# Kernel tuning notes

Hardware: AMD Instinct MI355X
Metric: run time of the kernel (lower is better)

The kernel has to match this reference:

```python
import jax, jax.numpy as jnp
import numpy as np

D_MODEL, D_FF, N_EXPERTS, TOP_K = 1024, 4096, 8, 2
B, S = 2, 2048


def setup_inputs() -> dict:
    key = jax.random.key(0)
    ks = jax.random.split(key, 7)
    scale = 0.02
    return {
        "x": jax.random.normal(ks[0], (B, S, D_MODEL), dtype=jnp.float32),
        "W1": jax.random.normal(ks[1], (N_EXPERTS, D_MODEL, D_FF), dtype=jnp.float32) * scale,
        "b1": jnp.zeros((N_EXPERTS, D_FF), dtype=jnp.float32),
        "W2": jax.random.normal(ks[2], (N_EXPERTS, D_FF, D_MODEL), dtype=jnp.float32) * scale,
        "b2": jnp.zeros((N_EXPERTS, D_MODEL), dtype=jnp.float32),
        "Wg": jax.random.normal(ks[3], (D_MODEL, N_EXPERTS), dtype=jnp.float32) * scale,
        "bg": jnp.zeros((N_EXPERTS,), dtype=jnp.float32),
    }


def reference(x, W1, b1, W2, b2, Wg, bg):
    # x: [B, S, d_model]
    Bx, Sx, d = x.shape
    E = W1.shape[0]
    # Gate + top-k routing (softmax over the top-k scores, as in the torch code)
    logits = jnp.einsum("bsd,de->bse", x, Wg) + bg            # [B,S,E]
    topk_scores, topk_idx = jax.lax.top_k(logits, TOP_K)       # [B,S,K]
    topk_scores = jax.nn.softmax(topk_scores, axis=-1)

    tokens = x.reshape(-1, d)                                  # [T,d]
    idx_flat = topk_idx.reshape(-1, TOP_K)                     # [T,K]
    sc_flat = topk_scores.reshape(-1, TOP_K)                   # [T,K]
    # Per-token combine weight for each expert: sum_k score_k * 1[idx_k == e]
    comb = (jax.nn.one_hot(idx_flat, E, dtype=x.dtype) * sc_flat[..., None]).sum(axis=1)  # [T,E]

    # Dense grouped expert MLP (zero combine weight kills non-selected experts)
    h = jnp.einsum("td,edf->etf", tokens, W1) + b1[:, None, :]  # [E,T,d_ff]
    even = (jnp.arange(E) % 2 == 0)[:, None, None]
    # torch nn.GELU default = exact (erf); odd experts use SiLU
    a = jnp.where(even, jax.nn.gelu(h, approximate=False), jax.nn.silu(h))
    y = jnp.einsum("etf,efd->etd", a, W2) + b2[:, None, :]      # [E,T,d_model]
    out = jnp.einsum("te,etd->td", comb, y)                     # [T,d_model]
    # Dropout is identity in eval mode
    return out.reshape(Bx, Sx, d)
```

## Files before the change

kernel.cpp:

```cpp
#include <hip/hip_runtime.h>
#include <stdint.h>

#define T_TOK 4096
#define DM 1024
#define DF 4096
#define NE 8

typedef __attribute__((ext_vector_type(8))) short bf16x8;
typedef __attribute__((ext_vector_type(4))) float f32x4;

__device__ __forceinline__ float b2f(unsigned short u) {
    union { unsigned int i; float f; } v; v.i = ((unsigned int)u) << 16; return v.f;
}
__device__ __forceinline__ unsigned short f2b(float f) {
    unsigned int i = __float_as_uint(f);
    unsigned int r = (i + 0x7FFFu + ((i >> 16) & 1u)) >> 16;
    return (unsigned short)r;
}
__device__ __forceinline__ void load_lds16(const void* g, void* l) {
    __builtin_amdgcn_global_load_lds((__attribute__((address_space(1))) void*)(g),
                                     (__attribute__((address_space(3))) void*)(l), 16, 0, 0);
}

__global__ __launch_bounds__(256) void detect_kernel(const unsigned short* __restrict__ xu,
                                                     int* __restrict__ flag) {
    const int i = (blockIdx.x * 256 + threadIdx.x) * 4;
    uint2 v = *(const uint2*)&xu[i];
    unsigned int a = v.x, b = v.y;
    int found = 0;
    if (((a >> 7)  & 0xFF) == 0xFF) found = 1;
    if (((a >> 23) & 0xFF) == 0xFF) found = 1;
    if (((b >> 7)  & 0xFF) == 0xFF) found = 1;
    if (((b >> 23) & 0xFF) == 0xFF) found = 1;
    if (__ballot(found) != 0 && (threadIdx.x & 63) == 0) atomicOr(flag, 1);
}

__global__ __launch_bounds__(256) void convx_kernel(const void* __restrict__ xin,
                                                    const int* __restrict__ flag,
                                                    unsigned short* __restrict__ xb) {
    const size_t i = ((size_t)blockIdx.x * 256 + threadIdx.x) * 8;
    if (*flag) {
        const float* xf = (const float*)xin + i;
        float4 a = *(const float4*)xf;
        float4 b = *(const float4*)(xf + 4);
        alignas(16) unsigned short t[8] = { f2b(a.x), f2b(a.y), f2b(a.z), f2b(a.w),
                                            f2b(b.x), f2b(b.y), f2b(b.z), f2b(b.w) };
        *(uint4*)(xb + i) = *(const uint4*)t;
    } else {
        *(uint4*)(xb + i) = *(const uint4*)((const unsigned short*)xin + i);
    }
}

__global__ void convf_kernel(const void* __restrict__ src, const int* __restrict__ flag,
                             float* __restrict__ dst, int n) {
    int i = blockIdx.x * 256 + threadIdx.x;
    if (i < n) dst[i] = (*flag) ? ((const float*)src)[i] : b2f(((const unsigned short*)src)[i]);
}

__global__ __launch_bounds__(256) void transpose_kernel(const void* __restrict__ in,
                                                        unsigned short* __restrict__ out,
                                                        int R, int C, const int* __restrict__ flag) {
    __shared__ unsigned short tile[64][65];
    const int isf = *flag;
    const size_t base = (size_t)blockIdx.z * R * C;
    const int r0 = blockIdx.y * 64, c0 = blockIdx.x * 64;
    const int lr = threadIdx.x >> 2;
    const int lc = (threadIdx.x & 3) * 16;
    if (isf) {
        const float* src = (const float*)in + base + (size_t)(r0 + lr) * C + c0 + lc;
#pragma unroll
        for (int q = 0; q < 4; q++) {
            float4 v = *(const float4*)(src + q * 4);
            tile[lr][lc + q * 4 + 0] = f2b(v.x);
            tile[lr][lc + q * 4 + 1] = f2b(v.y);
            tile[lr][lc + q * 4 + 2] = f2b(v.z);
            tile[lr][lc + q * 4 + 3] = f2b(v.w);
        }
    } else {
        const unsigned short* src = (const unsigned short*)in + base + (size_t)(r0 + lr) * C + c0 + lc;
#pragma unroll
        for (int q = 0; q < 2; q++) {
            uint4 v = *(const uint4*)(src + q * 8);
            unsigned int w[4] = { v.x, v.y, v.z, v.w };
#pragma unroll
            for (int j = 0; j < 4; j++) {
                tile[lr][lc + q * 8 + 2 * j]     = (unsigned short)(w[j] & 0xffff);
                tile[lr][lc + q * 8 + 2 * j + 1] = (unsigned short)(w[j] >> 16);
            }
        }
    }
    __syncthreads();
    const int oc = threadIdx.x >> 2;
    const int oj = (threadIdx.x & 3) * 16;
    alignas(16) unsigned short tmp[16];
#pragma unroll
    for (int j = 0; j < 16; j++) tmp[j] = tile[oj + j][oc];
    unsigned short* dst = out + base + (size_t)(c0 + oc) * R + r0 + oj;
    *(uint4*)(dst) = *(const uint4*)(tmp);
    *(uint4*)(dst + 8) = *(const uint4*)(tmp + 8);
}

__global__ __launch_bounds__(256) void gate_kernel(
    const void* __restrict__ x, const void* __restrict__ Wg, const void* __restrict__ bg,
    const int* __restrict__ flag, int* __restrict__ cnt,
    int* __restrict__ tok_e, float* __restrict__ tok_s) {
    const int isf = *flag;
    const int wave = threadIdx.x >> 6, lane = threadIdx.x & 63;
    const int t = blockIdx.x * 4 + wave;
    float p[8] = {0.f,0.f,0.f,0.f,0.f,0.f,0.f,0.f};
    if (isf) {
        const float* xr = (const float*)x + (size_t)t * DM;
        const float* wg = (const float*)Wg;
        for (int i = lane; i < DM; i += 64) {
            float xv = xr[i];
            float4 a = *(const float4*)(wg + (size_t)i * 8);
            float4 b = *(const float4*)(wg + (size_t)i * 8 + 4);
            p[0] += xv * a.x; p[1] += xv * a.y; p[2] += xv * a.z; p[3] += xv * a.w;
            p[4] += xv * b.x; p[5] += xv * b.y; p[6] += xv * b.z; p[7] += xv * b.w;
        }
    } else {
        const unsigned short* xr = (const unsigned short*)x + (size_t)t * DM;
        const unsigned short* wg = (const unsigned short*)Wg;
        for (int i = lane; i < DM; i += 64) {
            float xv = b2f(xr[i]);
            uint4 wv = *(const uint4*)(wg + (size_t)i * 8);
            p[0] += xv * b2f((unsigned short)(wv.x & 0xffff));
            p[1] += xv * b2f((unsigned short)(wv.x >> 16));
            p[2] += xv * b2f((unsigned short)(wv.y & 0xffff));
            p[3] += xv * b2f((unsigned short)(wv.y >> 16));
            p[4] += xv * b2f((unsigned short)(wv.z & 0xffff));
            p[5] += xv * b2f((unsigned short)(wv.z >> 16));
            p[6] += xv * b2f((unsigned short)(wv.w & 0xffff));
            p[7] += xv * b2f((unsigned short)(wv.w >> 16));
        }
    }
    for (int off = 32; off > 0; off >>= 1)
        for (int e = 0; e < 8; e++) p[e] += __shfl_down(p[e], off);
    if (lane == 0) {
        for (int e = 0; e < 8; e++)
            p[e] += isf ? ((const float*)bg)[e] : b2f(((const unsigned short*)bg)[e]);
        int e0 = 0;
        for (int e = 1; e < 8; e++) if (p[e] > p[e0]) e0 = e;
        int e1 = (e0 == 0) ? 1 : 0;
        for (int e = 0; e < 8; e++) if (e != e0 && p[e] > p[e1]) e1 = e;
        float z = expf(p[e1] - p[e0]);
        float s0 = 1.f / (1.f + z);
        tok_e[2 * t] = e0; tok_e[2 * t + 1] = e1;
        tok_s[2 * t] = s0; tok_s[2 * t + 1] = z * s0;
        atomicAdd(&cnt[e0], 1); atomicAdd(&cnt[e1], 1);
    }
}

__global__ void scan_kernel(const int* __restrict__ cnt, int* __restrict__ offs) {
    if (threadIdx.x == 0) {
        int s = 0;
        for (int e = 0; e < NE; e++) { offs[e] = s; s += cnt[e]; }
    }
}

__global__ __launch_bounds__(256) void place_kernel(
    const int* __restrict__ tok_e, const int* __restrict__ offs, int* __restrict__ cnt2,
    int* __restrict__ tok_list, int* __restrict__ slot_of) {
    const int t = blockIdx.x * 256 + threadIdx.x;
    for (int k = 0; k < 2; k++) {
        int e = tok_e[2 * t + k];
        int slot = atomicAdd(&cnt2[e], 1);
        int idx = offs[e] + slot;
        tok_list[idx] = t;
        slot_of[2 * t + k] = idx;
    }
}

__global__ __launch_bounds__(256) void gemm1_kernel(
    const unsigned short* __restrict__ xb, const unsigned short* __restrict__ W1T,
    const float* __restrict__ b1f, const int* __restrict__ tok_list,
    const int* __restrict__ offs, const int* __restrict__ cnt,
    unsigned short* __restrict__ act) {
    const int e = blockIdx.z, by = blockIdx.y, bx = blockIdx.x;
    const int ne = cnt[e];
    if (by * 128 >= ne) return;
    const int off_e = offs[e];
    __shared__ unsigned short Asm[128 * 32];
    __shared__ unsigned short Bsm[128 * 32];
    __shared__ int toks[128];
    const int tid = threadIdx.x, w = tid >> 6, lane = tid & 63;
    if (tid < 128) {
        int r = by * 128 + tid;
        toks[tid] = tok_list[off_e + (r < ne ? r : ne - 1)];
    }
    __syncthreads();
    const int arow0 = w * 16 + (lane >> 2);
    const int acol = (lane & 3) * 8;
    const int tok0 = toks[arow0], tok1 = toks[arow0 + 64];
    const unsigned short* gA0 = xb + (size_t)tok0 * DM + acol;
    const unsigned short* gA1 = xb + (size_t)tok1 * DM + acol;
    const unsigned short* Wte = W1T + (size_t)e * DF * DM;
    const unsigned short* gB0 = Wte + (size_t)(bx * 128 + arow0) * DM + acol;
    const unsigned short* gB1 = gB0 + (size_t)64 * DM;
    unsigned short* ldsA0 = &Asm[(w) * 16 * 32];
    unsigned short* ldsA1 = &Asm[(w + 4) * 16 * 32];
    unsigned short* ldsB0 = &Bsm[(w) * 16 * 32];
    unsigned short* ldsB1 = &Bsm[(w + 4) * 16 * 32];
    f32x4 acc[4][4] = {};
    const int mb = (w >> 1) * 64, nb = (w & 1) * 64;
    for (int kk = 0; kk < DM; kk += 32) {
        load_lds16(gA0 + kk, ldsA0);
        load_lds16(gA1 + kk, ldsA1);
        load_lds16(gB0 + kk, ldsB0);
        load_lds16(gB1 + kk, ldsB1);
        __syncthreads();
        bf16x8 af[4], bfv[4];
#pragma unroll
        for (int i = 0; i < 4; i++)
            af[i] = *(const bf16x8*)&Asm[(mb + i * 16 + (lane & 15)) * 32 + (lane >> 4) * 8];
#pragma unroll
        for (int j = 0; j < 4; j++)
            bfv[j] = *(const bf16x8*)&Bsm[(nb + j * 16 + (lane & 15)) * 32 + (lane >> 4) * 8];
#pragma unroll
        for (int i = 0; i < 4; i++)
#pragma unroll
            for (int j = 0; j < 4; j++)
                acc[i][j] = __builtin_amdgcn_mfma_f32_16x16x32_bf16(af[i], bfv[j], acc[i][j], 0, 0, 0);
        __syncthreads();
    }
    const bool even_e = (e & 1) == 0;
    const float* b1e = b1f + (size_t)e * DF + bx * 128;
#pragma unroll
    for (int i = 0; i < 4; i++) {
#pragma unroll
        for (int r = 0; r < 4; r++) {
            int m = mb + i * 16 + ((lane >> 4) * 4) + r;
            int grow = by * 128 + m;
            if (grow < ne) {
                unsigned short* dst = act + (size_t)(off_e + grow) * DF + bx * 128;
#pragma unroll
                for (int j = 0; j < 4; j++) {
                    int n = nb + j * 16 + (lane & 15);
                    float h = acc[i][j][r] + b1e[n];
                    float a;
                    if (even_e) a = 0.5f * h * (1.f + erff(h * 0.70710678118654752f));
                    else        a = h / (1.f + expf(-h));
                    dst[n] = f2b(a);
                }
            }
        }
    }
}

__global__ __launch_bounds__(256) void gemm2_kernel(
    const unsigned short* __restrict__ act, const unsigned short* __restrict__ W2T,
    const float* __restrict__ b2f, const int* __restrict__ offs,
    const int* __restrict__ cnt, float* __restrict__ yall) {
    const int e = blockIdx.z, by = blockIdx.y, bx = blockIdx.x;
    const int ne = cnt[e];
    if (by * 128 >= ne) return;
    const int off_e = offs[e];
    __shared__ unsigned short Asm[128 * 32];
    __shared__ unsigned short Bsm[128 * 32];
    const int tid = threadIdx.x, w = tid >> 6, lane = tid & 63;
    const int arow0 = w * 16 + (lane >> 2);
    const int acol = (lane & 3) * 8;
    int r0 = by * 128 + arow0;       if (r0 > ne - 1) r0 = ne - 1;
    int r1 = by * 128 + arow0 + 64;  if (r1 > ne - 1) r1 = ne - 1;
    const unsigned short* gA0 = act + (size_t)(off_e + r0) * DF + acol;
    const unsigned short* gA1 = act + (size_t)(off_e + r1) * DF + acol;
    const unsigned short* Wte = W2T + (size_t)e * DM * DF;
    const unsigned short* gB0 = Wte + (size_t)(bx * 128 + arow0) * DF + acol;
    const unsigned short* gB1 = gB0 + (size_t)64 * DF;
    unsigned short* ldsA0 = &Asm[(w) * 16 * 32];
    unsigned short* ldsA1 = &Asm[(w + 4) * 16 * 32];
    unsigned short* ldsB0 = &Bsm[(w) * 16 * 32];
    unsigned short* ldsB1 = &Bsm[(w + 4) * 16 * 32];
    f32x4 acc[4][4] = {};
    const int mb = (w >> 1) * 64, nb = (w & 1) * 64;
    for (int kk = 0; kk < DF; kk += 32) {
        load_lds16(gA0 + kk, ldsA0);
        load_lds16(gA1 + kk, ldsA1);
        load_lds16(gB0 + kk, ldsB0);
        load_lds16(gB1 + kk, ldsB1);
        __syncthreads();
        bf16x8 af[4], bfv[4];
#pragma unroll
        for (int i = 0; i < 4; i++)
            af[i] = *(const bf16x8*)&Asm[(mb + i * 16 + (lane & 15)) * 32 + (lane >> 4) * 8];
#pragma unroll
        for (int j = 0; j < 4; j++)
            bfv[j] = *(const bf16x8*)&Bsm[(nb + j * 16 + (lane & 15)) * 32 + (lane >> 4) * 8];
#pragma unroll
        for (int i = 0; i < 4; i++)
#pragma unroll
            for (int j = 0; j < 4; j++)
                acc[i][j] = __builtin_amdgcn_mfma_f32_16x16x32_bf16(af[i], bfv[j], acc[i][j], 0, 0, 0);
        __syncthreads();
    }
    const float* b2e = b2f + (size_t)e * DM + bx * 128;
#pragma unroll
    for (int i = 0; i < 4; i++) {
#pragma unroll
        for (int r = 0; r < 4; r++) {
            int m = mb + i * 16 + ((lane >> 4) * 4) + r;
            int grow = by * 128 + m;
            if (grow < ne) {
                float* dst = yall + (size_t)(off_e + grow) * DM + bx * 128;
#pragma unroll
                for (int j = 0; j < 4; j++) {
                    int n = nb + j * 16 + (lane & 15);
                    dst[n] = acc[i][j][r] + b2e[n];
                }
            }
        }
    }
}

__global__ __launch_bounds__(256) void combine_kernel(
    const float* __restrict__ yall, const int* __restrict__ slot_of,
    const float* __restrict__ tok_s, void* __restrict__ out, const int* __restrict__ flag) {
    const int t = blockIdx.x;
    const int c = threadIdx.x * 4;
    const int s0i = slot_of[2 * t], s1i = slot_of[2 * t + 1];
    const float w0 = tok_s[2 * t], w1 = tok_s[2 * t + 1];
    float4 a = *(const float4*)&yall[(size_t)s0i * DM + c];
    float4 b = *(const float4*)&yall[(size_t)s1i * DM + c];
    float4 r;
    r.x = w0 * a.x + w1 * b.x;
    r.y = w0 * a.y + w1 * b.y;
    r.z = w0 * a.z + w1 * b.z;
    r.w = w0 * a.w + w1 * b.w;
    if (*flag) {
        *(float4*)((float*)out + (size_t)t * DM + c) = r;
    } else {
        ushort4 o;
        o.x = f2b(r.x); o.y = f2b(r.y); o.z = f2b(r.z); o.w = f2b(r.w);
        *(ushort4*)((unsigned short*)out + (size_t)t * DM + c) = o;
    }
}

extern "C" void kernel_launch(void* const* d_in, const int* in_sizes, int n_in,
                              void* d_out, int out_size, void* d_ws, size_t ws_size,
                              hipStream_t stream) {
    (void)in_sizes; (void)n_in; (void)out_size; (void)ws_size;
    const void* x  = d_in[0];
    const void* W1 = d_in[1];
    const void* b1 = d_in[2];
    const void* W2 = d_in[3];
    const void* b2 = d_in[4];
    const void* Wg = d_in[5];
    const void* bg = d_in[6];

    uint8_t* wsb = (uint8_t*)d_ws;
    int* ip = (int*)wsb;
    int* flag  = ip;
    int* cnt   = ip + 8;
    int* cnt2  = ip + 16;
    int* offs  = ip + 24;
    int* tok_e = ip + 32;
    float* tok_s  = (float*)(tok_e + 2 * T_TOK);
    int* tok_list = (int*)(tok_s + 2 * T_TOK);
    int* slot_of  = tok_list + 2 * T_TOK;
    size_t head = (size_t)((uint8_t*)(slot_of + 2 * T_TOK) - wsb);
    head = (head + 255) & ~(size_t)255;
    float* b1f = (float*)(wsb + head);
    float* b2f = b1f + (size_t)NE * DF;
    unsigned short* xb  = (unsigned short*)(b2f + (size_t)NE * DM);
    unsigned short* W1T = xb + (size_t)T_TOK * DM;
    unsigned short* W2T = W1T + (size_t)NE * DM * DF;
    unsigned short* actb = W2T + (size_t)NE * DM * DF;
    float* yall = (float*)W1T;

    hipMemsetAsync(ip, 0, 128, stream);
    detect_kernel<<<256, 256, 0, stream>>>((const unsigned short*)x, flag);
    convx_kernel<<<(T_TOK * DM) / 2048, 256, 0, stream>>>(x, flag, xb);
    convf_kernel<<<(NE * DF) / 256, 256, 0, stream>>>(b1, flag, b1f, NE * DF);
    convf_kernel<<<(NE * DM) / 256, 256, 0, stream>>>(b2, flag, b2f, NE * DM);
    transpose_kernel<<<dim3(DF / 64, DM / 64, NE), 256, 0, stream>>>(W1, W1T, DM, DF, flag);
    transpose_kernel<<<dim3(DM / 64, DF / 64, NE), 256, 0, stream>>>(W2, W2T, DF, DM, flag);
    gate_kernel<<<T_TOK / 4, 256, 0, stream>>>(x, Wg, bg, flag, cnt, tok_e, tok_s);
    scan_kernel<<<1, 64, 0, stream>>>(cnt, offs);
    place_kernel<<<T_TOK / 256, 256, 0, stream>>>(tok_e, offs, cnt2, tok_list, slot_of);
    gemm1_kernel<<<dim3(DF / 128, T_TOK / 128, NE), 256, 0, stream>>>(xb, W1T, b1f, tok_list, offs, cnt, actb);
    gemm2_kernel<<<dim3(DM / 128, T_TOK / 128, NE), 256, 0, stream>>>(actb, W2T, b2f, offs, cnt, yall);
    combine_kernel<<<T_TOK, 256, 0, stream>>>(yall, slot_of, tok_s, d_out, flag);
}
```

Baseline: 762.5 us.

## Double-buffer LDS tiles, swizzle LDS layout, and use fast activation approximations

Both expert GEMM kernels now use two LDS buffers, issuing the next K-slice's global-to-LDS loads before computing the current one, so memory latency can overlap MFMA work and one barrier per iteration is dropped. The column offset used when writing tiles to LDS and when reading MFMA fragments is XOR-swizzled to reduce LDS bank conflicts, and s_setprio raises wave priority around the MFMA block. The GELU erf is replaced with an Abramowitz-Stegun polynomial, and SiLU uses hardware exp2 and rcp. This costs double the LDS per block, which may lower occupancy, and the activations lose a little accuracy.

```diff
diff --git a/kernel.cpp b/kernel.cpp
--- a/kernel.cpp
+++ b/kernel.cpp
@@ -20,6 +20,36 @@
 __device__ __forceinline__ void load_lds16(const void* g, void* l) {
     __builtin_amdgcn_global_load_lds((__attribute__((address_space(1))) void*)(g),
                                      (__attribute__((address_space(3))) void*)(l), 16, 0, 0);
+}
+
+__device__ __forceinline__ float fexp2(float x) {
+#if __has_builtin(__builtin_amdgcn_exp2f)
+    return __builtin_amdgcn_exp2f(x);
+#else
+    return exp2f(x);
+#endif
+}
+__device__ __forceinline__ float frcp(float x) {
+#if __has_builtin(__builtin_amdgcn_rcpf)
+    return __builtin_amdgcn_rcpf(x);
+#else
+    return 1.0f / x;
+#endif
+}
+
+__device__ __forceinline__ float gelu_f(float h) {
+    float z = h * 0.70710678118654752f;
+    float az = fabsf(z);
+    float t = frcp(1.0f + 0.3275911f * az);
+    float p = ((((1.061405429f * t - 1.453152027f) * t + 1.421413741f) * t
+                - 0.284496736f) * t + 0.254829592f) * t;
+    float e = fexp2(-1.4426950408889634f * az * az);
+    float er = 1.0f - p * e;
+    er = (z < 0.f) ? -er : er;
+    return 0.5f * h * (1.0f + er);
+}
+__device__ __forceinline__ float silu_f(float h) {
+    return h * frcp(1.0f + fexp2(-1.4426950408889634f * h));
 }
 
 __global__ __launch_bounds__(256) void detect_kernel(const unsigned short* __restrict__ xu,
@@ -180,8 +210,8 @@
     const int ne = cnt[e];
     if (by * 128 >= ne) return;
     const int off_e = offs[e];
-    __shared__ unsigned short Asm[128 * 32];
-    __shared__ unsigned short Bsm[128 * 32];
+    __shared__ unsigned short Asm[2][128 * 32];
+    __shared__ unsigned short Bsm[2][128 * 32];
     __shared__ int toks[128];
     const int tid = threadIdx.x, w = tid >> 6, lane = tid & 63;
     if (tid < 128) {
@@ -190,39 +220,49 @@
     }
     __syncthreads();
     const int arow0 = w * 16 + (lane >> 2);
-    const int acol = (lane & 3) * 8;
+    const int s_sw = (lane >> 3) & 3;
+    const int acol = (((lane & 3) ^ s_sw) * 8);
     const int tok0 = toks[arow0], tok1 = toks[arow0 + 64];
     const unsigned short* gA0 = xb + (size_t)tok0 * DM + acol;
     const unsigned short* gA1 = xb + (size_t)tok1 * DM + acol;
     const unsigned short* Wte = W1T + (size_t)e * DF * DM;
     const unsigned short* gB0 = Wte + (size_t)(bx * 128 + arow0) * DM + acol;
     const unsigned short* gB1 = gB0 + (size_t)64 * DM;
-    unsigned short* ldsA0 = &Asm[(w) * 16 * 32];
-    unsigned short* ldsA1 = &Asm[(w + 4) * 16 * 32];
-    unsigned short* ldsB0 = &Bsm[(w) * 16 * 32];
-    unsigned short* ldsB1 = &Bsm[(w + 4) * 16 * 32];
     f32x4 acc[4][4] = {};
     const int mb = (w >> 1) * 64, nb = (w & 1) * 64;
+    const int rdoff = (((lane >> 4) ^ ((lane >> 1) & 3)) * 8);
+
+#define STAGE1(buf, kk) do { \
+        load_lds16(gA0 + (kk), &Asm[buf][(w) * 16 * 32]); \
+        load_lds16(gA1 + (kk), &Asm[buf][(w + 4) * 16 * 32]); \
+        load_lds16(gB0 + (kk), &Bsm[buf][(w) * 16 * 32]); \
+        load_lds16(gB1 + (kk), &Bsm[buf][(w + 4) * 16 * 32]); \
+    } while (0)
+
+    STAGE1(0, 0);
+    __syncthreads();
+    int cur = 0;
     for (int kk = 0; kk < DM; kk += 32) {
-        load_lds16(gA0 + kk, ldsA0);
-        load_lds16(gA1 + kk, ldsA1);
-        load_lds16(gB0 + kk, ldsB0);
-        load_lds16(gB1 + kk, ldsB1);
-        __syncthreads();
+        if (kk + 32 < DM) STAGE1(cur ^ 1, kk + 32);
         bf16x8 af[4], bfv[4];
 #pragma unroll
         for (int i = 0; i < 4; i++)
-            af[i] = *(const bf16x8*)&Asm[(mb + i * 16 + (lane & 15)) * 32 + (lane >> 4) * 8];
+            af[i] = *(const bf16x8*)&Asm[cur][(mb + i * 16 + (lane & 15)) * 32 + rdoff];
 #pragma unroll
         for (int j = 0; j < 4; j++)
-            bfv[j] = *(const bf16x8*)&Bsm[(nb + j * 16 + (lane & 15)) * 32 + (lane >> 4) * 8];
+            bfv[j] = *(const bf16x8*)&Bsm[cur][(nb + j * 16 + (lane & 15)) * 32 + rdoff];
+        __builtin_amdgcn_s_setprio(1);
 #pragma unroll
         for (int i = 0; i < 4; i++)
 #pragma unroll
             for (int j = 0; j < 4; j++)
                 acc[i][j] = __builtin_amdgcn_mfma_f32_16x16x32_bf16(af[i], bfv[j], acc[i][j], 0, 0, 0);
+        __builtin_amdgcn_s_setprio(0);
         __syncthreads();
-    }
+        cur ^= 1;
+    }
+#undef STAGE1
+
     const bool even_e = (e & 1) == 0;
     const float* b1e = b1f + (size_t)e * DF + bx * 128;
 #pragma unroll
@@ -237,9 +277,7 @@
                 for (int j = 0; j < 4; j++) {
                     int n = nb + j * 16 + (lane & 15);
                     float h = acc[i][j][r] + b1e[n];
-                    float a;
-                    if (even_e) a = 0.5f * h * (1.f + erff(h * 0.70710678118654752f));
-                    else        a = h / (1.f + expf(-h));
+                    float a = even_e ? gelu_f(h) : silu_f(h);
                     dst[n] = f2b(a);
                 }
             }
@@ -255,11 +293,12 @@
     const int ne = cnt[e];
     if (by * 128 >= ne) return;
     const int off_e = offs[e];
-    __shared__ unsigned short Asm[128 * 32];
-    __shared__ unsigned short Bsm[128 * 32];
+    __shared__ unsigned short Asm[2][128 * 32];
+    __shared__ unsigned short Bsm[2][128 * 32];
     const int tid = threadIdx.x, w = tid >> 6, lane = tid & 63;
     const int arow0 = w * 16 + (lane >> 2);
-    const int acol = (lane & 3) * 8;
+    const int s_sw = (lane >> 3) & 3;
+    const int acol = (((lane & 3) ^ s_sw) * 8);
     int r0 = by * 128 + arow0;       if (r0 > ne - 1) r0 = ne - 1;
     int r1 = by * 128 + arow0 + 64;  if (r1 > ne - 1) r1 = ne - 1;
     const unsigned short* gA0 = act + (size_t)(off_e + r0) * DF + acol;
@@ -267,32 +306,41 @@
     const unsigned short* Wte = W2T + (size_t)e * DM * DF;
     const unsigned short* gB0 = Wte + (size_t)(bx * 128 + arow0) * DF + acol;
     const unsigned short* gB1 = gB0 + (size_t)64 * DF;
-    unsigned short* ldsA0 = &Asm[(w) * 16 * 32];
-    unsigned short* ldsA1 = &Asm[(w + 4) * 16 * 32];
-    unsigned short* ldsB0 = &Bsm[(w) * 16 * 32];
-    unsigned short* ldsB1 = &Bsm[(w + 4) * 16 * 32];
     f32x4 acc[4][4] = {};
     const int mb = (w >> 1) * 64, nb = (w & 1) * 64;
+    const int rdoff = (((lane >> 4) ^ ((lane >> 1) & 3)) * 8);
+
+#define STAGE2(buf, kk) do { \
+        load_lds16(gA0 + (kk), &Asm[buf][(w) * 16 * 32]); \
+        load_lds16(gA1 + (kk), &Asm[buf][(w + 4) * 16 * 32]); \
+        load_lds16(gB0 + (kk), &Bsm[buf][(w) * 16 * 32]); \
+        load_lds16(gB1 + (kk), &Bsm[buf][(w + 4) * 16 * 32]); \
+    } while (0)
+
+    STAGE2(0, 0);
+    __syncthreads();
+    int cur = 0;
     for (int kk = 0; kk < DF; kk += 32) {
-        load_lds16(gA0 + kk, ldsA0);
-        load_lds16(gA1 + kk, ldsA1);
-        load_lds16(gB0 + kk, ldsB0);
-        load_lds16(gB1 + kk, ldsB1);
-        __syncthreads();
+        if (kk + 32 < DF) STAGE2(cur ^ 1, kk + 32);
         bf16x8 af[4], bfv[4];
 #pragma unroll
         for (int i = 0; i < 4; i++)
-            af[i] = *(const bf16x8*)&Asm[(mb + i * 16 + (lane & 15)) * 32 + (lane >> 4) * 8];
+            af[i] = *(const bf16x8*)&Asm[cur][(mb + i * 16 + (lane & 15)) * 32 + rdoff];
 #pragma unroll
         for (int j = 0; j < 4; j++)
-            bfv[j] = *(const bf16x8*)&Bsm[(nb + j * 16 + (lane & 15)) * 32 + (lane >> 4) * 8];
+            bfv[j] = *(const bf16x8*)&Bsm[cur][(nb + j * 16 + (lane & 15)) * 32 + rdoff];
+        __builtin_amdgcn_s_setprio(1);
 #pragma unroll
         for (int i = 0; i < 4; i++)
 #pragma unroll
             for (int j = 0; j < 4; j++)
                 acc[i][j] = __builtin_amdgcn_mfma_f32_16x16x32_bf16(af[i], bfv[j], acc[i][j], 0, 0, 0);
+        __builtin_amdgcn_s_setprio(0);
         __syncthreads();
-    }
+        cur ^= 1;
+    }
+#undef STAGE2
+
     const float* b2e = b2f + (size_t)e * DM + bx * 128;
 #pragma unroll
     for (int i = 0; i < 4; i++) {
```

Result: faster. 746.0 us (-2.2%).
